# Kernel optimization log

Hardware: AMD Instinct MI355X
Metric: run time of the kernel (lower is better)

Reference implementation:

```python
import jax, jax.numpy as jnp
from jax import lax
import numpy as np

EPS_START, EPS_END, EPS_DECAY = 1.0, 0.05, 10000.0


def gru_step(x, h, w_ih, w_hh, b_ih, b_hh):
    # PyTorch GRUCell math; gates stacked as [r, z, n]
    gi = x @ w_ih.T + b_ih
    gh = h @ w_hh.T + b_hh
    i_r, i_z, i_n = jnp.split(gi, 3, axis=1)
    h_r, h_z, h_n = jnp.split(gh, 3, axis=1)
    r = jax.nn.sigmoid(i_r + h_r)
    z = jax.nn.sigmoid(i_z + h_z)
    n = jnp.tanh(i_n + r * h_n)
    return (1.0 - z) * n + z * h


def setup_inputs() -> dict:
    key = jax.random.key(0)
    ks = jax.random.split(key, 7)
    V, E, H = 32000, 256, 512
    s = 0.05
    return {
        "embedding": jax.random.normal(ks[0], (V, E), jnp.float32) * s,
        "w_ih": jax.random.normal(ks[1], (3 * H, E), jnp.float32) * s,
        "w_hh": jax.random.normal(ks[2], (3 * H, H), jnp.float32) * s,
        "b_ih": jax.random.normal(ks[3], (3 * H,), jnp.float32) * s,
        "b_hh": jax.random.normal(ks[4], (3 * H,), jnp.float32) * s,
        "w_out": jax.random.normal(ks[5], (V, H), jnp.float32) * s,
        "b_out": jax.random.normal(ks[6], (V,), jnp.float32) * s,
        "seq_len": 256,
        "batch_size": 512,
    }


def reference(embedding, w_ih, w_hh, b_ih, b_hh, w_out, b_out, seq_len, batch_size):
    V, E = embedding.shape
    H = w_hh.shape[1]
    B = batch_size
    log_unif = jnp.float32(np.log(V))  # -log(vocab_size) fill for epsilon-greedy

    keys = jax.random.split(jax.random.key(42), seq_len)
    ts = jnp.arange(seq_len, dtype=jnp.float32)

    h0 = jnp.zeros((B, H), jnp.float32)
    x0 = jnp.broadcast_to(embedding[0], (B, E))  # start token id 0

    def step(carry, inp):
        h, x = carry
        t, k = inp
        k_eps, k_gum = jax.random.split(k)
        h = gru_step(x, h, w_ih, w_hh, b_ih, b_hh)
        logp = jax.nn.log_softmax(h @ w_out.T + b_out, axis=1)  # [B, V]
        eps_t = EPS_END + (EPS_START - EPS_END) * jnp.exp(-4.0 * t / EPS_DECAY)
        draw = eps_t >= jax.random.uniform(k_eps, (B,))
        masked = jnp.where(draw[:, None], -log_unif, logp)
        g = jax.random.gumbel(k_gum, (B, V), jnp.float32)
        sampled = jnp.argmax(masked + g, axis=1)  # [B] int
        lp = jnp.take_along_axis(logp, sampled[:, None], axis=1)[:, 0]
        x_next = embedding[sampled]
        return (h, x_next), (sampled, lp)

    _, (samples, lps) = lax.scan(step, (h0, x0), (ts, keys))
    return samples.T, lps.T  # [B, S] each
```

## Files before the change

kernel.cpp:

```cpp
#include <hip/hip_runtime.h>
#include <math.h>
#include <stdio.h>

#ifndef JAX_PARTITIONABLE
#define JAX_PARTITIONABLE 1
#endif

namespace {

constexpr int B  = 512;
constexpr int S  = 256;
constexpr int E  = 256;
constexpr int H  = 512;
constexpr int V  = 32000;
constexpr int G3 = 3 * H;
constexpr int VBLK = 64;
constexpr int NCH  = V / VBLK;
constexpr int NDMAX = 96;

typedef __bf16 bf16x8 __attribute__((ext_vector_type(8)));
typedef float  f32x4  __attribute__((ext_vector_type(4)));
typedef unsigned u32x4 __attribute__((ext_vector_type(4)));

__device__ __forceinline__ void tf2x32(unsigned k0, unsigned k1,
                                       unsigned x0, unsigned x1,
                                       unsigned& o0, unsigned& o1) {
  unsigned ks2 = k0 ^ k1 ^ 0x1BD11BDAu;
  x0 += k0; x1 += k1;
#define TFR(r) { x0 += x1; x1 = (x1 << (r)) | (x1 >> (32 - (r))); x1 ^= x0; }
  TFR(13) TFR(15) TFR(26) TFR(6)   x0 += k1;  x1 += ks2 + 1u;
  TFR(17) TFR(29) TFR(16) TFR(24)  x0 += ks2; x1 += k0 + 2u;
  TFR(13) TFR(15) TFR(26) TFR(6)   x0 += k0;  x1 += k1 + 3u;
  TFR(17) TFR(29) TFR(16) TFR(24)  x0 += k1;  x1 += ks2 + 4u;
  TFR(13) TFR(15) TFR(26) TFR(6)   x0 += ks2; x1 += k0 + 5u;
#undef TFR
  o0 = x0; o1 = x1;
}

__device__ __forceinline__ unsigned rbits(unsigned g0, unsigned g1,
                                          unsigned b, unsigned v) {
#if JAX_PARTITIONABLE
  unsigned y0, y1;
  tf2x32(g0, g1, 0u, b * (unsigned)V + v, y0, y1);
  return y0 ^ y1;
#else
  const unsigned N2 = (unsigned)(B/2) * (unsigned)V;
  unsigned ii = b * (unsigned)V + v;
  unsigned jj = (b < 256) ? ii : ii - N2;
  unsigned y0, y1;
  tf2x32(g0, g1, jj, N2 + jj, y0, y1);
  return (b < 256) ? y0 : y1;
#endif
}

__device__ __forceinline__ float u01_from_bits(unsigned bits) {
  return __uint_as_float(0x3f800000u | (bits >> 9)) - 1.0f;
}

__device__ __forceinline__ float gumbel_exact(unsigned bits) {
  float u = u01_from_bits(bits);
  if (u == 0.0f) u = 1.1754943508222875e-38f;
  float w = (float)(-log((double)u));
  return (float)(-log((double)w));
}

__device__ __forceinline__ float gumbel_fast(unsigned bits) {
  float u = u01_from_bits(bits);
  if (u == 0.0f) u = 1.1754943508222875e-38f;
  float w = -__logf(u);
  return -__logf(w);
}

__device__ __forceinline__ unsigned short f2bf(float f) {
  unsigned u = __float_as_uint(f);
  unsigned r = (u + 0x7fffu + ((u >> 16) & 1u)) >> 16;
  return (unsigned short)r;
}

__device__ __forceinline__ size_t frag_off(int row, int k, int kTiles) {
  return ((size_t)((row >> 4) * kTiles + (k >> 5)) * 64
          + (row & 15) + 16 * ((k >> 3) & 3)) * 8 + (k & 7);
}

__global__ void k_init_rng(unsigned* __restrict__ kq, unsigned* __restrict__ ke) {
  int t = threadIdx.x;
  unsigned h0, h1, e0, e1, g0, g1;
#if JAX_PARTITIONABLE
  tf2x32(0u, 42u, 0u, (unsigned)t, h0, h1);
  tf2x32(h0, h1, 0u, 0u, e0, e1);
  tf2x32(h0, h1, 0u, 1u, g0, g1);
#else
  unsigned a0, a1, b0, b1;
  if (t < 128) {
    tf2x32(0u, 42u, (unsigned)(2*t),   (unsigned)(256+2*t), a0, a1);
    tf2x32(0u, 42u, (unsigned)(2*t+1), (unsigned)(257+2*t), b0, b1);
    h0 = a0; h1 = b0;
  } else {
    int j = 2*t - 256;
    tf2x32(0u, 42u, (unsigned)j,     (unsigned)(256+j), a0, a1);
    tf2x32(0u, 42u, (unsigned)(j+1), (unsigned)(257+j), b0, b1);
    h0 = a1; h1 = b1;
  }
  unsigned p0, p1, q0, q1;
  tf2x32(h0, h1, 0u, 2u, p0, p1);
  tf2x32(h0, h1, 1u, 3u, q0, q1);
  e0 = p0; e1 = q0; g0 = p1; g1 = q1;
#endif
  ke[2*t] = e0; ke[2*t+1] = e1;
  kq[2*t] = g0; kq[2*t+1] = g1;
}

__global__ void k_init_draws(const unsigned* __restrict__ ke,
                             unsigned char* __restrict__ draws) {
  int t = blockIdx.x;
  int b = threadIdx.x;
  unsigned k0 = ke[2*t], k1 = ke[2*t+1];
  unsigned bits, y0, y1;
#if JAX_PARTITIONABLE
  tf2x32(k0, k1, 0u, (unsigned)b, y0, y1);
  bits = y0 ^ y1;
#else
  if (b < 256) { tf2x32(k0, k1, (unsigned)b,       (unsigned)(256+b), y0, y1); bits = y0; }
  else         { tf2x32(k0, k1, (unsigned)(b-256), (unsigned)b,       y0, y1); bits = y1; }
#endif
  float u   = u01_from_bits(bits);
  float tf  = (float)t;
  float ex  = expf(__fmul_rn(-4.0f, tf) / 10000.0f);
  float eps = __fadd_rn(0.05f, __fmul_rn(0.95f, ex));
  draws[t*B + b] = (eps >= u) ? 1 : 0;
}

__global__ void k_init_nd(const unsigned char* __restrict__ draws,
                          int* __restrict__ nd_slot) {
  int t = blockIdx.x;
  if (threadIdx.x != 0) return;
  int cnt = 0;
  for (int b = 0; b < B; b++) {
    if (!draws[t*B + b] && cnt < NDMAX) nd_slot[t*B + b] = cnt++;
    else nd_slot[t*B + b] = -1;
  }
}

__global__ __launch_bounds__(256) void k_pre_argmax(
    const unsigned* __restrict__ kq, const unsigned char* __restrict__ draws,
    int* __restrict__ pre) {
  const int job  = blockIdx.x * 4 + (threadIdx.x >> 6);
  const int lane = threadIdx.x & 63;
  const int t = job >> 9, b = job & (B - 1);
  if (!draws[t*B + b]) { if (lane == 0) pre[job] = -1; return; }
  const unsigned g0 = kq[2*t], g1 = kq[2*t+1];
  unsigned best = 0u; int bv = V;
  for (int v = lane; v < V; v += 64) {
    unsigned bits = rbits(g0, g1, (unsigned)b, (unsigned)v) >> 9;
    if (bits > best || (bits == best && v < bv)) { best = bits; bv = v; }
  }
#pragma unroll
  for (int m = 1; m < 64; m <<= 1) {
    unsigned ob = __shfl_xor(best, m, 64);
    int      ov = __shfl_xor(bv,   m, 64);
    if (ob > best || (ob == best && ov < bv)) { best = ob; bv = ov; }
  }
  if (lane == 0) pre[job] = bv;
}

__global__ void k_init_state(const float* __restrict__ emb,
                             float* __restrict__ x, float* __restrict__ h) {
  int b = blockIdx.x, tid = threadIdx.x;
  x[b*E + tid] = emb[tid];
  h[b*H + tid] = 0.0f;
  h[b*H + 256 + tid] = 0.0f;
}

__global__ void k_cast_w(const float* __restrict__ w,
                         unsigned short* __restrict__ w_sw) {
  int g = blockIdx.x*256 + threadIdx.x;
  int v  = g >> 6;
  int k0 = (g & 63) * 8;
  const float* src = w + (size_t)v*H + k0;
  union { unsigned short s[8]; u32x4 vv; } u;
#pragma unroll
  for (int e = 0; e < 8; e++) u.s[e] = f2bf(src[e]);
  *(u32x4*)&w_sw[frag_off(v, k0, H/32)] = u.vv;
}

__global__ __launch_bounds__(512) void k_gates(
    const float* __restrict__ x, const float* __restrict__ h,
    const float* __restrict__ w_ih, const float* __restrict__ w_hh,
    const float* __restrict__ b_ih, const float* __restrict__ b_hh,
    float* __restrict__ gi, float* __restrict__ gh) {
  const int z = blockIdx.z;
  const float* A    = z ? h    : x;
  const float* W    = z ? w_hh : w_ih;
  const float* bias = z ? b_hh : b_ih;
  float*       C    = z ? gh   : gi;
  const int K       = z ? H    : E;

  __shared__ __align__(16) float As[16][68];
  __shared__ __align__(16) float Ws[16][68];
  const int tid = threadIdx.x;
  const int tx = tid & 15, ty = tid >> 4;
  const int row0 = blockIdx.y * 64, col0 = blockIdx.x * 64;
  float acc[2][4] = {};
  for (int k0 = 0; k0 < K; k0 += 16) {
#pragma unroll
    for (int l = 0; l < 2; l++) {
      int idx = tid + l*512;
      int r = idx >> 4, kk = idx & 15;
      As[kk][r] = A[(row0 + r)*K + k0 + kk];
      Ws[kk][r] = W[(col0 + r)*K + k0 + kk];
    }
    __syncthreads();
#pragma unroll
    for (int kk = 0; kk < 16; kk++) {
      const float2 av = *(const float2*)&As[kk][ty*2];
      const float4 wv = *(const float4*)&Ws[kk][tx*4];
      const float a[2] = {av.x, av.y};
      const float w[4] = {wv.x, wv.y, wv.z, wv.w};
#pragma unroll
      for (int i = 0; i < 2; i++)
#pragma unroll
        for (int j = 0; j < 4; j++) acc[i][j] = fmaf(a[i], w[j], acc[i][j]);
    }
    __syncthreads();
  }
#pragma unroll
  for (int i = 0; i < 2; i++) {
    int r = row0 + ty*2 + i;
    int c = col0 + tx*4;
    float4 o;
    o.x = __fadd_rn(acc[i][0], bias[c + 0]);
    o.y = __fadd_rn(acc[i][1], bias[c + 1]);
    o.z = __fadd_rn(acc[i][2], bias[c + 2]);
    o.w = __fadd_rn(acc[i][3], bias[c + 3]);
    *(float4*)&C[r*G3 + c] = o;
  }
}

__device__ __forceinline__ float sigm_acc(float v) {
  return (float)(1.0 / (1.0 + exp(-(double)v)));
}
__device__ __forceinline__ float tanh_acc(float v) {
  return (float)tanh((double)v);
}

__global__ void k_gru_update(const float* __restrict__ gi,
                             const float* __restrict__ gh,
                             float* __restrict__ h,
                             unsigned short* __restrict__ h_sw) {
  int g = blockIdx.x*256 + threadIdx.x;
  int b  = g >> 6;
  int j0 = (g & 63) * 8;
  const float* gib = gi + (size_t)b*G3;
  const float* ghb = gh + (size_t)b*G3;
  float hn[8];
  union { unsigned short s[8]; u32x4 vv; } u;
#pragma unroll
  for (int e = 0; e < 8; e++) {
    int j = j0 + e;
    float r  = sigm_acc(__fadd_rn(gib[j],     ghb[j]));
    float zz = sigm_acc(__fadd_rn(gib[H+j],   ghb[H+j]));
    float nn = tanh_acc(__fadd_rn(gib[2*H+j], __fmul_rn(r, ghb[2*H+j])));
    float hv = h[(size_t)b*H + j];
    float t1 = __fmul_rn(__fsub_rn(1.0f, zz), nn);
    float t2 = __fmul_rn(zz, hv);
    hn[e] = __fadd_rn(t1, t2);
    u.s[e] = f2bf(hn[e]);
  }
#pragma unroll
  for (int e = 0; e < 8; e++) h[(size_t)b*H + j0 + e] = hn[e];
  *(u32x4*)&h_sw[frag_off(b, j0, H/32)] = u.vv;
}

__global__ __launch_bounds__(256) void k_mfma_logits(
    const unsigned short* __restrict__ h_sw,
    const unsigned short* __restrict__ w_sw,
    const float* __restrict__ b_out,
    const unsigned* __restrict__ kq,
    const unsigned char* __restrict__ draws,
    int* __restrict__ pre,
    const int* __restrict__ nd_slot_t,
    float* __restrict__ pmax, float* __restrict__ psum,
    float* __restrict__ plog,
    float* __restrict__ nd_keys, float* __restrict__ nd_kmax, int t) {
  const int tid  = threadIdx.x;

  if (blockIdx.y == 0) {
    __shared__ unsigned sb[4];
    __shared__ int      sv[4];
    const int tn = t + 1;
    if (tn >= S) return;
    const int b = blockIdx.x;
    if (!draws[tn*B + b]) { if (tid == 0) pre[tn*B + b] = -1; return; }
    const unsigned g0 = kq[2*tn], g1 = kq[2*tn+1];
    unsigned best = 0u; int bv = V;
    for (int v = tid; v < V; v += 256) {
      unsigned bits = rbits(g0, g1, (unsigned)b, (unsigned)v) >> 9;
      if (bits > best || (bits == best && v < bv)) { best = bits; bv = v; }
    }
#pragma unroll
    for (int m = 1; m < 64; m <<= 1) {
      unsigned ob = __shfl_xor(best, m, 64);
      int      ov = __shfl_xor(bv,   m, 64);
      if (ob > best || (ob == best && ov < bv)) { best = ob; bv = ov; }
    }
    const int wv = tid >> 6;
    if ((tid & 63) == 0) { sb[wv] = best; sv[wv] = bv; }
    __syncthreads();
    if (tid == 0) {
      for (int i = 1; i < 4; i++) {
        unsigned ob = sb[i]; int ov = sv[i];
        if (ob > best || (ob == best && ov < bv)) { best = ob; bv = ov; }
      }
      pre[tn*B + b] = bv;
    }
    return;
  }

  const int L  = (blockIdx.y - 1) * 512 + blockIdx.x;
  const int wg = (L & 7) * 128 + (L >> 3);
  if (wg >= 2*NCH) return;
  const int vblk = wg >> 1;
  const int bblk = wg & 1;
  const int* __restrict__ pre_t = pre + t*B;
  const int lane = tid & 63, w = tid >> 6;
  const int quad = lane >> 4, l15 = lane & 15;

  f32x4 acc[4][4] = {};

  const int mtBase = bblk*16 + w*4;
  const int ntBase = vblk*4;
  const unsigned short* hp = h_sw + (size_t)mtBase*16*512 + lane*8;
  const unsigned short* wp = w_sw + (size_t)ntBase*16*512 + lane*8;

  bf16x8 afc[4], bfc[4];
#pragma unroll
  for (int mt = 0; mt < 4; mt++)
    afc[mt] = __builtin_bit_cast(bf16x8, *(const u32x4*)(hp + (size_t)(mt*16)*512));
#pragma unroll
  for (int nt = 0; nt < 4; nt++)
    bfc[nt] = __builtin_bit_cast(bf16x8, *(const u32x4*)(wp + (size_t)(nt*16)*512));

#pragma unroll 1
  for (int kt = 0; kt < 15; kt++) {
    bf16x8 afn[4], bfn[4];
#pragma unroll
    for (int mt = 0; mt < 4; mt++)
      afn[mt] = __builtin_bit_cast(bf16x8,
          *(const u32x4*)(hp + (size_t)(mt*16 + kt + 1)*512));
#pragma unroll
    for (int nt = 0; nt < 4; nt++)
      bfn[nt] = __builtin_bit_cast(bf16x8,
          *(const u32x4*)(wp + (size_t)(nt*16 + kt + 1)*512));
#pragma unroll
    for (int mt = 0; mt < 4; mt++)
#pragma unroll
      for (int nt = 0; nt < 4; nt++)
        acc[mt][nt] = __builtin_amdgcn_mfma_f32_16x16x32_bf16(
            afc[mt], bfc[nt], acc[mt][nt], 0, 0, 0);
#pragma unroll
    for (int mt = 0; mt < 4; mt++) afc[mt] = afn[mt];
#pragma unroll
    for (int nt = 0; nt < 4; nt++) bfc[nt] = bfn[nt];
  }
  {
#pragma unroll
    for (int mt = 0; mt < 4; mt++)
#pragma unroll
      for (int nt = 0; nt < 4; nt++)
        acc[mt][nt] = __builtin_amdgcn_mfma_f32_16x16x32_bf16(
            afc[mt], bfc[nt], acc[mt][nt], 0, 0, 0);
  }

  const int bW = bblk*256 + w*64;
  const int vW = vblk*64;
  const unsigned g0 = kq[2*t], g1 = kq[2*t+1];
  float bias[4];
#pragma unroll
  for (int nt = 0; nt < 4; nt++) bias[nt] = b_out[vW + nt*16 + l15];

#pragma unroll
  for (int mt = 0; mt < 4; mt++) {
#pragma unroll
    for (int r = 0; r < 4; r++) {
      const int b = bW + mt*16 + quad*4 + r;
      float lg[4];
#pragma unroll
      for (int nt = 0; nt < 4; nt++) lg[nt] = acc[mt][nt][r] + bias[nt];
      float lmax = fmaxf(fmaxf(lg[0], lg[1]), fmaxf(lg[2], lg[3]));
#pragma unroll
      for (int m = 1; m < 16; m <<= 1) lmax = fmaxf(lmax, __shfl_xor(lmax, m, 64));
      float ls = 0.0f;
#pragma unroll
      for (int nt = 0; nt < 4; nt++) ls += __expf(lg[nt] - lmax);
#pragma unroll
      for (int m = 1; m < 16; m <<= 1) ls += __shfl_xor(ls, m, 64);
      if (l15 == 0) { pmax[b*NCH + vblk] = lmax; psum[b*NCH + vblk] = ls; }
      const int pr = pre_t[b];
      if (pr >= 0) {
        int rel = pr - vW;
        if (rel >= 0 && rel < 64 && (rel & 15) == l15) plog[b] = lg[rel >> 4];
      } else {
        const int slot = nd_slot_t[b];
        if (slot >= 0) {
          float key[4];
#pragma unroll
          for (int nt = 0; nt < 4; nt++)
            key[nt] = lg[nt] + gumbel_fast(
                rbits(g0, g1, (unsigned)b, (unsigned)(vW + nt*16 + l15)));
          float* dst = nd_keys + (size_t)slot*V + vW + l15;
#pragma unroll
          for (int nt = 0; nt < 4; nt++) dst[nt*16] = key[nt];
          float kmx = fmaxf(fmaxf(key[0], key[1]), fmaxf(key[2], key[3]));
#pragma unroll
          for (int m = 1; m < 16; m <<= 1) kmx = fmaxf(kmx, __shfl_xor(kmx, m, 64));
          if (l15 == 0) nd_kmax[slot*NCH + vblk] = kmx;
        }
      }
    }
  }
}

__global__ __launch_bounds__(256) void k_finish(
    const float* __restrict__ pmax, const float* __restrict__ psum,
    const float* __restrict__ plog,
    const int* __restrict__ pre_t, const int* __restrict__ nd_slot_t,
    const float* __restrict__ nd_keys, const float* __restrict__ nd_kmax,
    const unsigned* __restrict__ kq,
    const float* __restrict__ h, const float* __restrict__ w_out,
    const float* __restrict__ b_out,
    const float* __restrict__ emb, float* __restrict__ x,
    float* __restrict__ out_samples, float* __restrict__ out_lps, int t) {
  const int b = blockIdx.x;
  const int tid = threadIdx.x;
  __shared__ float sA[256];
  __shared__ int   cand[160];
  __shared__ float cand_key[160], cand_lg[160];
  __shared__ int   ccnt;
  __shared__ int   s_samp;
  __shared__ float s_blog;

  float m = -INFINITY;
  for (int c = tid; c < NCH; c += 256) m = fmaxf(m, pmax[b*NCH + c]);
  sA[tid] = m; __syncthreads();
  for (int s = 128; s > 0; s >>= 1) {
    if (tid < s) sA[tid] = fmaxf(sA[tid], sA[tid+s]);
    __syncthreads();
  }
  const float M = sA[0];
  __syncthreads();
  float sum = 0.0f;
  for (int c = tid; c < NCH; c += 256)
    sum += psum[b*NCH + c] * expf(pmax[b*NCH + c] - M);
  sA[tid] = sum; __syncthreads();
  for (int s = 128; s > 0; s >>= 1) {
    if (tid < s) sA[tid] += sA[tid+s];
    __syncthreads();
  }
  const float SUM = sA[0];
  __syncthreads();

  const int pr = pre_t[b];
  if (pr >= 0) {
    if (tid == 0) { s_samp = pr; s_blog = plog[b]; }
  } else {
    const int slot = nd_slot_t[b];
    if (slot < 0) {
      if (tid == 0) { s_samp = 0; s_blog = plog[b]; }
    } else {
      const unsigned g0 = kq[2*t], g1 = kq[2*t+1];
      if (tid == 0) ccnt = 0;
      float km = -INFINITY;
      for (int c = tid; c < NCH; c += 256) km = fmaxf(km, nd_kmax[slot*NCH + c]);
      sA[tid] = km; __syncthreads();
      for (int s = 128; s > 0; s >>= 1) {
        if (tid < s) sA[tid] = fmaxf(sA[tid], sA[tid+s]);
        __syncthreads();
      }
      const float thr = sA[0] - 0.0859375f;
      __syncthreads();
      const float* keys = nd_keys + (size_t)slot*V;
      for (int c = tid; c < NCH; c += 256) {
        if (nd_kmax[slot*NCH + c] >= thr) {
          for (int j = 0; j < VBLK; j++) {
            float k = keys[c*VBLK + j];
            if (k >= thr) {
              int p = atomicAdd(&ccnt, 1);
              if (p < 160) cand[p] = c*VBLK + j;
            }
          }
        }
      }
      __syncthreads();
      const int nc = min(ccnt, 160);
      const int wid = tid >> 6, lane = tid & 63;
      for (int c = wid; c < nc; c += 4) {
        const int v = cand[c];
        const float* wr = w_out + (size_t)v*H;
        const float* hr = h + (size_t)b*H;
        float s = 0.0f;
#pragma unroll
        for (int i = 0; i < 8; i++) s = fmaf(hr[lane + 64*i], wr[lane + 64*i], s);
#pragma unroll
        for (int mm = 1; mm < 64; mm <<= 1) s += __shfl_xor(s, mm, 64);
        if (lane == 0) {
          float logit = __fadd_rn(s, b_out[v]);
          float key   = __fadd_rn(logit,
                          gumbel_exact(rbits(g0, g1, (unsigned)b, (unsigned)v)));
          cand_key[c] = key; cand_lg[c] = logit;
        }
      }
      __syncthreads();
      if (tid == 0) {
        float bk = -INFINITY; int bv = V; float bl = 0.0f;
        for (int c = 0; c < nc; c++) {
          float k = cand_key[c]; int v = cand[c];
          if (k > bk || (k == bk && v < bv)) { bk = k; bv = v; bl = cand_lg[c]; }
        }
        s_samp = bv; s_blog = bl;
      }
    }
  }
  __syncthreads();
  const int sampled = s_samp;
  if (tid == 0) {
    float lse = (float)log((double)SUM);
    float lp  = __fsub_rn(__fsub_rn(s_blog, M), lse);
    out_samples[b*S + t] = (float)sampled;
    out_lps[b*S + t]     = lp;
  }
  x[b*E + tid] = emb[sampled*E + tid];
}

}

extern "C" void kernel_launch(void* const* d_in, const int* in_sizes, int n_in,
                              void* d_out, int out_size, void* d_ws, size_t ws_size,
                              hipStream_t stream) {
  (void)in_sizes; (void)n_in; (void)out_size;
  const float* emb   = (const float*)d_in[0];
  const float* w_ih  = (const float*)d_in[1];
  const float* w_hh  = (const float*)d_in[2];
  const float* b_ih  = (const float*)d_in[3];
  const float* b_hh  = (const float*)d_in[4];
  const float* w_out = (const float*)d_in[5];
  const float* b_out = (const float*)d_in[6];
  float* out = (float*)d_out;

  char* wsb = (char*)d_ws;
  size_t off = 0;
  auto alloc = [&](size_t nbytes) {
    char* p = wsb + off;
    off += (nbytes + 255) & ~size_t(255);
    return p;
  };
  float* h     = (float*)alloc((size_t)B*H*4);
  float* x     = (float*)alloc((size_t)B*E*4);
  float* gi    = (float*)alloc((size_t)B*G3*4);
  float* gh    = (float*)alloc((size_t)B*G3*4);
  unsigned short* h_sw = (unsigned short*)alloc((size_t)B*H*2);
  unsigned short* w_sw = (unsigned short*)alloc((size_t)V*H*2);
  float* pmax  = (float*)alloc((size_t)B*NCH*4);
  float* psum  = (float*)alloc((size_t)B*NCH*4);
  float* plog  = (float*)alloc((size_t)B*4);
  unsigned* kq = (unsigned*)alloc((size_t)S*2*4);
  unsigned* ke = (unsigned*)alloc((size_t)S*2*4);
  unsigned char* draws = (unsigned char*)alloc((size_t)S*B);
  int* pre     = (int*)alloc((size_t)S*B*4);
  int* nd_slot = (int*)alloc((size_t)S*B*4);
  float* nd_keys = (float*)alloc((size_t)NDMAX*V*4);
  float* nd_kmax = (float*)alloc((size_t)NDMAX*NCH*4);
  if (off > ws_size) {
    fprintf(stderr, "kernel_launch: workspace too small (need %zu, have %zu)\n",
            off, ws_size);
    return;
  }

  k_init_rng<<<1, S, 0, stream>>>(kq, ke);
  k_init_draws<<<S, B, 0, stream>>>(ke, draws);
  k_init_nd<<<S, 64, 0, stream>>>(draws, nd_slot);
  k_pre_argmax<<<B/4, 256, 0, stream>>>(kq, draws, pre);
  k_init_state<<<B, 256, 0, stream>>>(emb, x, h);
  k_cast_w<<<(V*H/8)/256, 256, 0, stream>>>(w_out, w_sw);

  for (int t = 0; t < S; t++) {
    k_gates<<<dim3(G3/64, B/64, 2), 512, 0, stream>>>(x, h, w_ih, w_hh,
                                                      b_ih, b_hh, gi, gh);
    k_gru_update<<<(B*H/8)/256, 256, 0, stream>>>(gi, gh, h, h_sw);
    k_mfma_logits<<<dim3(512, 3), 256, 0, stream>>>(
        h_sw, w_sw, b_out, kq, draws, pre, nd_slot + t*B,
        pmax, psum, plog, nd_keys, nd_kmax, t);
    k_finish<<<B, 256, 0, stream>>>(pmax, psum, plog, pre + t*B, nd_slot + t*B,
                                    nd_keys, nd_kmax, kq, h, w_out, b_out,
                                    emb, x, out, out + (size_t)B*S, t);
  }
}
```

Before: 35.87 ms.

## Fuse GRU gate GEMMs with the GRU update and ping-pong hidden state

The separate gate GEMM kernel and GRU update kernel become one kernel. Each block computes the r, z and n gate columns for 8 hidden units over 64 batch rows, then applies the GRU nonlinearity directly, so the gi/gh intermediates never round-trip through global memory and one launch per step is removed. The hidden state is double-buffered so a block can read the old h while others write the new one. The cost is a smaller per-block tile (8 columns x 3 gates) with less register reuse. Each thread also writes scalar bf16 stores to the swizzled buffer instead of 16-byte vector stores.

```diff
diff --git a/kernel.cpp b/kernel.cpp
--- a/kernel.cpp
+++ b/kernel.cpp
@@ -13,7 +13,6 @@
 constexpr int E  = 256;
 constexpr int H  = 512;
 constexpr int V  = 32000;
-constexpr int G3 = 3 * H;
 constexpr int VBLK = 64;
 constexpr int NCH  = V / VBLK;
 constexpr int NDMAX = 96;
@@ -183,92 +182,107 @@
   *(u32x4*)&w_sw[frag_off(v, k0, H/32)] = u.vv;
 }
 
-__global__ __launch_bounds__(512) void k_gates(
-    const float* __restrict__ x, const float* __restrict__ h,
+__device__ __forceinline__ float sigm_acc(float v) {
+  return (float)(1.0 / (1.0 + exp(-(double)v)));
+}
+__device__ __forceinline__ float tanh_acc(float v) {
+  return (float)tanh((double)v);
+}
+
+__global__ __launch_bounds__(256) void k_gates_gru(
+    const float* __restrict__ x, const float* __restrict__ hin,
     const float* __restrict__ w_ih, const float* __restrict__ w_hh,
     const float* __restrict__ b_ih, const float* __restrict__ b_hh,
-    float* __restrict__ gi, float* __restrict__ gh) {
-  const int z = blockIdx.z;
-  const float* A    = z ? h    : x;
-  const float* W    = z ? w_hh : w_ih;
-  const float* bias = z ? b_hh : b_ih;
-  float*       C    = z ? gh   : gi;
-  const int K       = z ? H    : E;
-
+    float* __restrict__ hout, unsigned short* __restrict__ h_sw) {
   __shared__ __align__(16) float As[16][68];
-  __shared__ __align__(16) float Ws[16][68];
+  __shared__ __align__(16) float Ws[16][28];
   const int tid = threadIdx.x;
-  const int tx = tid & 15, ty = tid >> 4;
-  const int row0 = blockIdx.y * 64, col0 = blockIdx.x * 64;
-  float acc[2][4] = {};
-  for (int k0 = 0; k0 < K; k0 += 16) {
+  const int jj = tid & 7, ty = tid >> 3;
+  const int j0 = blockIdx.x * 8;
+  const int row0 = blockIdx.y * 64;
+  float ai[2][3] = {};
+  float ah[2][3] = {};
+
+  for (int k0 = 0; k0 < E; k0 += 16) {
+    __syncthreads();
+#pragma unroll
+    for (int l = 0; l < 4; l++) {
+      int idx = tid + l*256;
+      int r = idx >> 4, kk = idx & 15;
+      As[kk][r] = x[(size_t)(row0 + r)*E + k0 + kk];
+    }
 #pragma unroll
     for (int l = 0; l < 2; l++) {
-      int idx = tid + l*512;
+      int idx = tid + l*256;
+      if (idx < 384) {
+        int r = idx >> 4, kk = idx & 15;
+        int col = (r >> 3)*512 + j0 + (r & 7);
+        Ws[kk][r] = w_ih[(size_t)col*E + k0 + kk];
+      }
+    }
+    __syncthreads();
+#pragma unroll
+    for (int kk = 0; kk < 16; kk++) {
+      float a0 = As[kk][ty], a1 = As[kk][ty + 32];
+#pragma unroll
+      for (int g = 0; g < 3; g++) {
+        float w = Ws[kk][g*8 + jj];
+        ai[0][g] = fmaf(a0, w, ai[0][g]);
+        ai[1][g] = fmaf(a1, w, ai[1][g]);
+      }
+    }
+  }
+
+  for (int k0 = 0; k0 < H; k0 += 16) {
+    __syncthreads();
+#pragma unroll
+    for (int l = 0; l < 4; l++) {
+      int idx = tid + l*256;
       int r = idx >> 4, kk = idx & 15;
-      As[kk][r] = A[(row0 + r)*K + k0 + kk];
-      Ws[kk][r] = W[(col0 + r)*K + k0 + kk];
+      As[kk][r] = hin[(size_t)(row0 + r)*H + k0 + kk];
+    }
+#pragma unroll
+    for (int l = 0; l < 2; l++) {
+      int idx = tid + l*256;
+      if (idx < 384) {
+        int r = idx >> 4, kk = idx & 15;
+        int col = (r >> 3)*512 + j0 + (r & 7);
+        Ws[kk][r] = w_hh[(size_t)col*H + k0 + kk];
+      }
     }
     __syncthreads();
 #pragma unroll
     for (int kk = 0; kk < 16; kk++) {
-      const float2 av = *(const float2*)&As[kk][ty*2];
-      const float4 wv = *(const float4*)&Ws[kk][tx*4];
-      const float a[2] = {av.x, av.y};
-      const float w[4] = {wv.x, wv.y, wv.z, wv.w};
-#pragma unroll
-      for (int i = 0; i < 2; i++)
-#pragma unroll
-        for (int j = 0; j < 4; j++) acc[i][j] = fmaf(a[i], w[j], acc[i][j]);
-    }
-    __syncthreads();
-  }
+      float a0 = As[kk][ty], a1 = As[kk][ty + 32];
+#pragma unroll
+      for (int g = 0; g < 3; g++) {
+        float w = Ws[kk][g*8 + jj];
+        ah[0][g] = fmaf(a0, w, ah[0][g]);
+        ah[1][g] = fmaf(a1, w, ah[1][g]);
+      }
+    }
+  }
+
+  const int j = j0 + jj;
 #pragma unroll
   for (int i = 0; i < 2; i++) {
-    int r = row0 + ty*2 + i;
-    int c = col0 + tx*4;
-    float4 o;
-    o.x = __fadd_rn(acc[i][0], bias[c + 0]);
-    o.y = __fadd_rn(acc[i][1], bias[c + 1]);
-    o.z = __fadd_rn(acc[i][2], bias[c + 2]);
-    o.w = __fadd_rn(acc[i][3], bias[c + 3]);
-    *(float4*)&C[r*G3 + c] = o;
-  }
-}
-
-__device__ __forceinline__ float sigm_acc(float v) {
-  return (float)(1.0 / (1.0 + exp(-(double)v)));
-}
-__device__ __forceinline__ float tanh_acc(float v) {
-  return (float)tanh((double)v);
-}
-
-__global__ void k_gru_update(const float* __restrict__ gi,
-                             const float* __restrict__ gh,
-                             float* __restrict__ h,
-                             unsigned short* __restrict__ h_sw) {
-  int g = blockIdx.x*256 + threadIdx.x;
-  int b  = g >> 6;
-  int j0 = (g & 63) * 8;
-  const float* gib = gi + (size_t)b*G3;
-  const float* ghb = gh + (size_t)b*G3;
-  float hn[8];
-  union { unsigned short s[8]; u32x4 vv; } u;
-#pragma unroll
-  for (int e = 0; e < 8; e++) {
-    int j = j0 + e;
-    float r  = sigm_acc(__fadd_rn(gib[j],     ghb[j]));
-    float zz = sigm_acc(__fadd_rn(gib[H+j],   ghb[H+j]));
-    float nn = tanh_acc(__fadd_rn(gib[2*H+j], __fmul_rn(r, ghb[2*H+j])));
-    float hv = h[(size_t)b*H + j];
+    const int b = row0 + ty + i*32;
+    float gi_r = __fadd_rn(ai[i][0], b_ih[j]);
+    float gi_z = __fadd_rn(ai[i][1], b_ih[512 + j]);
+    float gi_n = __fadd_rn(ai[i][2], b_ih[1024 + j]);
+    float gh_r = __fadd_rn(ah[i][0], b_hh[j]);
+    float gh_z = __fadd_rn(ah[i][1], b_hh[512 + j]);
+    float gh_n = __fadd_rn(ah[i][2], b_hh[1024 + j]);
+    float r  = sigm_acc(__fadd_rn(gi_r, gh_r));
+    float zz = sigm_acc(__fadd_rn(gi_z, gh_z));
+    float nn = tanh_acc(__fadd_rn(gi_n, __fmul_rn(r, gh_n)));
+    float hv = hin[(size_t)b*H + j];
     float t1 = __fmul_rn(__fsub_rn(1.0f, zz), nn);
     float t2 = __fmul_rn(zz, hv);
-    hn[e] = __fadd_rn(t1, t2);
-    u.s[e] = f2bf(hn[e]);
-  }
-#pragma unroll
-  for (int e = 0; e < 8; e++) h[(size_t)b*H + j0 + e] = hn[e];
-  *(u32x4*)&h_sw[frag_off(b, j0, H/32)] = u.vv;
+    float hn = __fadd_rn(t1, t2);
+    hout[(size_t)b*H + j] = hn;
+    h_sw[frag_off(b, j, H/32)] = f2bf(hn);
+  }
 }
 
 __global__ __launch_bounds__(256) void k_mfma_logits(
@@ -553,10 +567,9 @@
     off += (nbytes + 255) & ~size_t(255);
     return p;
   };
-  float* h     = (float*)alloc((size_t)B*H*4);
+  float* h0    = (float*)alloc((size_t)B*H*4);
+  float* h1    = (float*)alloc((size_t)B*H*4);
   float* x     = (float*)alloc((size_t)B*E*4);
-  float* gi    = (float*)alloc((size_t)B*G3*4);
-  float* gh    = (float*)alloc((size_t)B*G3*4);
   unsigned short* h_sw = (unsigned short*)alloc((size_t)B*H*2);
   unsigned short* w_sw = (unsigned short*)alloc((size_t)V*H*2);
   float* pmax  = (float*)alloc((size_t)B*NCH*4);
@@ -579,18 +592,19 @@
   k_init_draws<<<S, B, 0, stream>>>(ke, draws);
   k_init_nd<<<S, 64, 0, stream>>>(draws, nd_slot);
   k_pre_argmax<<<B/4, 256, 0, stream>>>(kq, draws, pre);
-  k_init_state<<<B, 256, 0, stream>>>(emb, x, h);
+  k_init_state<<<B, 256, 0, stream>>>(emb, x, h0);
   k_cast_w<<<(V*H/8)/256, 256, 0, stream>>>(w_out, w_sw);
 
   for (int t = 0; t < S; t++) {
-    k_gates<<<dim3(G3/64, B/64, 2), 512, 0, stream>>>(x, h, w_ih, w_hh,
-                                                      b_ih, b_hh, gi, gh);
-    k_gru_update<<<(B*H/8)/256, 256, 0, stream>>>(gi, gh, h, h_sw);
+    float* hin  = (t & 1) ? h1 : h0;
+    float* hout = (t & 1) ? h0 : h1;
+    k_gates_gru<<<dim3(64, 8), 256, 0, stream>>>(x, hin, w_ih, w_hh,
+                                                 b_ih, b_hh, hout, h_sw);
     k_mfma_logits<<<dim3(512, 3), 256, 0, stream>>>(
         h_sw, w_sw, b_out, kq, draws, pre, nd_slot + t*B,
         pmax, psum, plog, nd_keys, nd_kmax, t);
     k_finish<<<B, 256, 0, stream>>>(pmax, psum, plog, pre + t*B, nd_slot + t*B,
-                                    nd_keys, nd_kmax, kq, h, w_out, b_out,
+                                    nd_keys, nd_kmax, kq, hout, w_out, b_out,
                                     emb, x, out, out + (size_t)B*S, t);
   }
 }
```

Measured after the change: 39.49 ms. 10.1% more time.

## Fuse GRU update and finish into preceding kernels via atomic last-block counters

Applied to the files above, without the earlier changes.

The GRU elementwise update moves into k_gates: the last of the 48 blocks to finish a 64-row batch slab, detected with an atomic counter, applies the gates for that slab. The finish/sampling stage moves into k_mfma_logits: the last 512 blocks to arrive spin until all blocks have written their partials, then each does the per-row reduction and sampling. This cuts two kernel launches per timestep, 512 launches in total. In exchange it needs relaxed atomic loads and stores for cross-block visibility, ping-pong h buffers, and a spin-wait whose forward progress depends on all blocks of the grid being resident or already retired.

```diff
diff --git a/kernel.cpp b/kernel.cpp
--- a/kernel.cpp
+++ b/kernel.cpp
@@ -21,6 +21,9 @@
 typedef __bf16 bf16x8 __attribute__((ext_vector_type(8)));
 typedef float  f32x4  __attribute__((ext_vector_type(4)));
 typedef unsigned u32x4 __attribute__((ext_vector_type(4)));
+
+#define AST(p, v) __hip_atomic_store((p), (v), __ATOMIC_RELAXED, __HIP_MEMORY_SCOPE_AGENT)
+#define ALD(p)    __hip_atomic_load((p), __ATOMIC_RELAXED, __HIP_MEMORY_SCOPE_AGENT)
 
 __device__ __forceinline__ void tf2x32(unsigned k0, unsigned k1,
                                        unsigned x0, unsigned x1,
@@ -82,8 +85,10 @@
           + (row & 15) + 16 * ((k >> 3) & 3)) * 8 + (k & 7);
 }
 
-__global__ void k_init_rng(unsigned* __restrict__ kq, unsigned* __restrict__ ke) {
+__global__ void k_init_rng(unsigned* __restrict__ kq, unsigned* __restrict__ ke,
+                           unsigned* __restrict__ ctrs) {
   int t = threadIdx.x;
+  ctrs[t] = 0u;
   unsigned h0, h1, e0, e1, g0, g1;
 #if JAX_PARTITIONABLE
   tf2x32(0u, 42u, 0u, (unsigned)t, h0, h1);
@@ -183,13 +188,22 @@
   *(u32x4*)&w_sw[frag_off(v, k0, H/32)] = u.vv;
 }
 
+__device__ __forceinline__ float sigm_acc(float v) {
+  return (float)(1.0 / (1.0 + exp(-(double)v)));
+}
+__device__ __forceinline__ float tanh_acc(float v) {
+  return (float)tanh((double)v);
+}
+
 __global__ __launch_bounds__(512) void k_gates(
-    const float* __restrict__ x, const float* __restrict__ h,
+    const float* __restrict__ x, const float* __restrict__ hin,
     const float* __restrict__ w_ih, const float* __restrict__ w_hh,
     const float* __restrict__ b_ih, const float* __restrict__ b_hh,
-    float* __restrict__ gi, float* __restrict__ gh) {
+    float* __restrict__ gi, float* __restrict__ gh,
+    float* __restrict__ hout, unsigned short* __restrict__ h_sw,
+    unsigned* __restrict__ ctrs, int t) {
   const int z = blockIdx.z;
-  const float* A    = z ? h    : x;
+  const float* A    = z ? hin  : x;
   const float* W    = z ? w_hh : w_ih;
   const float* bias = z ? b_hh : b_ih;
   float*       C    = z ? gh   : gi;
@@ -197,6 +211,7 @@
 
   __shared__ __align__(16) float As[16][68];
   __shared__ __align__(16) float Ws[16][68];
+  __shared__ unsigned s_old;
   const int tid = threadIdx.x;
   const int tx = tid & 15, ty = tid >> 4;
   const int row0 = blockIdx.y * 64, col0 = blockIdx.x * 64;
@@ -227,51 +242,41 @@
   for (int i = 0; i < 2; i++) {
     int r = row0 + ty*2 + i;
     int c = col0 + tx*4;
-    float4 o;
-    o.x = __fadd_rn(acc[i][0], bias[c + 0]);
-    o.y = __fadd_rn(acc[i][1], bias[c + 1]);
-    o.z = __fadd_rn(acc[i][2], bias[c + 2]);
-    o.w = __fadd_rn(acc[i][3], bias[c + 3]);
-    *(float4*)&C[r*G3 + c] = o;
-  }
-}
-
-__device__ __forceinline__ float sigm_acc(float v) {
-  return (float)(1.0 / (1.0 + exp(-(double)v)));
-}
-__device__ __forceinline__ float tanh_acc(float v) {
-  return (float)tanh((double)v);
-}
-
-__global__ void k_gru_update(const float* __restrict__ gi,
-                             const float* __restrict__ gh,
-                             float* __restrict__ h,
-                             unsigned short* __restrict__ h_sw) {
-  int g = blockIdx.x*256 + threadIdx.x;
-  int b  = g >> 6;
-  int j0 = (g & 63) * 8;
-  const float* gib = gi + (size_t)b*G3;
-  const float* ghb = gh + (size_t)b*G3;
-  float hn[8];
-  union { unsigned short s[8]; u32x4 vv; } u;
-#pragma unroll
-  for (int e = 0; e < 8; e++) {
-    int j = j0 + e;
-    float r  = sigm_acc(__fadd_rn(gib[j],     ghb[j]));
-    float zz = sigm_acc(__fadd_rn(gib[H+j],   ghb[H+j]));
-    float nn = tanh_acc(__fadd_rn(gib[2*H+j], __fmul_rn(r, ghb[2*H+j])));
-    float hv = h[(size_t)b*H + j];
+#pragma unroll
+    for (int j = 0; j < 4; j++)
+      AST(&C[(size_t)r*G3 + c + j], __fadd_rn(acc[i][j], bias[c + j]));
+  }
+
+  asm volatile("s_waitcnt vmcnt(0)" ::: "memory");
+  __syncthreads();
+  if (tid == 0)
+    s_old = __hip_atomic_fetch_add(&ctrs[blockIdx.y * 16], 1u,
+                                   __ATOMIC_RELAXED, __HIP_MEMORY_SCOPE_AGENT);
+  __syncthreads();
+  if (s_old != 48u * (unsigned)(t + 1) - 1u) return;
+
+  for (int el = tid; el < 64 * H; el += 512) {
+    const int b = row0 + (el >> 9);
+    const int j = el & (H - 1);
+    float gir = ALD(&gi[(size_t)b*G3 + j]);
+    float giz = ALD(&gi[(size_t)b*G3 + H + j]);
+    float gin = ALD(&gi[(size_t)b*G3 + 2*H + j]);
+    float ghr = ALD(&gh[(size_t)b*G3 + j]);
+    float ghz = ALD(&gh[(size_t)b*G3 + H + j]);
+    float ghn = ALD(&gh[(size_t)b*G3 + 2*H + j]);
+    float r  = sigm_acc(__fadd_rn(gir, ghr));
+    float zz = sigm_acc(__fadd_rn(giz, ghz));
+    float nn = tanh_acc(__fadd_rn(gin, __fmul_rn(r, ghn)));
+    float hv = hin[(size_t)b*H + j];
     float t1 = __fmul_rn(__fsub_rn(1.0f, zz), nn);
     float t2 = __fmul_rn(zz, hv);
-    hn[e] = __fadd_rn(t1, t2);
-    u.s[e] = f2bf(hn[e]);
-  }
-#pragma unroll
-  for (int e = 0; e < 8; e++) h[(size_t)b*H + j0 + e] = hn[e];
-  *(u32x4*)&h_sw[frag_off(b, j0, H/32)] = u.vv;
-}
-
-__global__ __launch_bounds__(256) void k_mfma_logits(
+    float hn = __fadd_rn(t1, t2);
+    hout[(size_t)b*H + j] = hn;
+    h_sw[frag_off(b, j, H/32)] = f2bf(hn);
+  }
+}
+
+__global__ __launch_bounds__(256, 2) void k_mfma_logits(
     const unsigned short* __restrict__ h_sw,
     const unsigned short* __restrict__ w_sw,
     const float* __restrict__ b_out,
@@ -281,12 +286,23 @@
     const int* __restrict__ nd_slot_t,
     float* __restrict__ pmax, float* __restrict__ psum,
     float* __restrict__ plog,
-    float* __restrict__ nd_keys, float* __restrict__ nd_kmax, int t) {
+    float* __restrict__ nd_keys, float* __restrict__ nd_kmax,
+    const float* __restrict__ h, const float* __restrict__ w_out,
+    const float* __restrict__ emb, float* __restrict__ x,
+    float* __restrict__ out_samples, float* __restrict__ out_lps,
+    unsigned* __restrict__ ctrs, int t) {
   const int tid  = threadIdx.x;
+  __shared__ unsigned sb[4];
+  __shared__ int      sv[4];
+  __shared__ unsigned s_old;
+  __shared__ float sA[256];
+  __shared__ int   cand[160];
+  __shared__ float cand_key[160], cand_lg[160];
+  __shared__ int   ccnt;
+  __shared__ int   s_samp;
+  __shared__ float s_blog;
 
   if (blockIdx.y == 0) {
-    __shared__ unsigned sb[4];
-    __shared__ int      sv[4];
     const int tn = t + 1;
     if (tn >= S) return;
     const int b = blockIdx.x;
@@ -319,216 +335,224 @@
   const int L  = (blockIdx.y - 1) * 512 + blockIdx.x;
   const int wg = (L & 7) * 128 + (L >> 3);
   if (wg >= 2*NCH) return;
-  const int vblk = wg >> 1;
-  const int bblk = wg & 1;
-  const int* __restrict__ pre_t = pre + t*B;
-  const int lane = tid & 63, w = tid >> 6;
-  const int quad = lane >> 4, l15 = lane & 15;
-
-  f32x4 acc[4][4] = {};
-
-  const int mtBase = bblk*16 + w*4;
-  const int ntBase = vblk*4;
-  const unsigned short* hp = h_sw + (size_t)mtBase*16*512 + lane*8;
-  const unsigned short* wp = w_sw + (size_t)ntBase*16*512 + lane*8;
-
-  bf16x8 afc[4], bfc[4];
-#pragma unroll
-  for (int mt = 0; mt < 4; mt++)
-    afc[mt] = __builtin_bit_cast(bf16x8, *(const u32x4*)(hp + (size_t)(mt*16)*512));
-#pragma unroll
-  for (int nt = 0; nt < 4; nt++)
-    bfc[nt] = __builtin_bit_cast(bf16x8, *(const u32x4*)(wp + (size_t)(nt*16)*512));
+  {
+    const int vblk = wg >> 1;
+    const int bblk = wg & 1;
+    const int* __restrict__ pre_t = pre + t*B;
+    const int lane = tid & 63, w = tid >> 6;
+    const int quad = lane >> 4, l15 = lane & 15;
+
+    f32x4 acc[4][4] = {};
+
+    const int mtBase = bblk*16 + w*4;
+    const int ntBase = vblk*4;
+    const unsigned short* hp = h_sw + (size_t)mtBase*16*512 + lane*8;
+    const unsigned short* wp = w_sw + (size_t)ntBase*16*512 + lane*8;
+
+    bf16x8 afc[4], bfc[4];
+#pragma unroll
+    for (int mt = 0; mt < 4; mt++)
+      afc[mt] = __builtin_bit_cast(bf16x8, *(const u32x4*)(hp + (size_t)(mt*16)*512));
+#pragma unroll
+    for (int nt = 0; nt < 4; nt++)
+      bfc[nt] = __builtin_bit_cast(bf16x8, *(const u32x4*)(wp + (size_t)(nt*16)*512));
 
 #pragma unroll 1
-  for (int kt = 0; kt < 15; kt++) {
-    bf16x8 afn[4], bfn[4];
-#pragma unroll
-    for (int mt = 0; mt < 4; mt++)
-      afn[mt] = __builtin_bit_cast(bf16x8,
-          *(const u32x4*)(hp + (size_t)(mt*16 + kt + 1)*512));
-#pragma unroll
-    for (int nt = 0; nt < 4; nt++)
-      bfn[nt] = __builtin_bit_cast(bf16x8,
-          *(const u32x4*)(wp + (size_t)(nt*16 + kt + 1)*512));
-#pragma unroll
-    for (int mt = 0; mt < 4; mt++)
+    for (int kt = 0; kt < 15; kt++) {
+      bf16x8 afn[4], bfn[4];
+#pragma unroll
+      for (int mt = 0; mt < 4; mt++)
+        afn[mt] = __builtin_bit_cast(bf16x8,
+            *(const u32x4*)(hp + (size_t)(mt*16 + kt + 1)*512));
 #pragma unroll
       for (int nt = 0; nt < 4; nt++)
-        acc[mt][nt] = __builtin_amdgcn_mfma_f32_16x16x32_bf16(
-            afc[mt], bfc[nt], acc[mt][nt], 0, 0, 0);
-#pragma unroll
-    for (int mt = 0; mt < 4; mt++) afc[mt] = afn[mt];
-#pragma unroll
-    for (int nt = 0; nt < 4; nt++) bfc[nt] = bfn[nt];
-  }
-  {
-#pragma unroll
-    for (int mt = 0; mt < 4; mt++)
-#pragma unroll
-      for (int nt = 0; nt < 4; nt++)
-        acc[mt][nt] = __builtin_amdgcn_mfma_f32_16x16x32_bf16(
-            afc[mt], bfc[nt], acc[mt][nt], 0, 0, 0);
-  }
-
-  const int bW = bblk*256 + w*64;
-  const int vW = vblk*64;
-  const unsigned g0 = kq[2*t], g1 = kq[2*t+1];
-  float bias[4];
-#pragma unroll
-  for (int nt = 0; nt < 4; nt++) bias[nt] = b_out[vW + nt*16 + l15];
-
-#pragma unroll
-  for (int mt = 0; mt < 4; mt++) {
-#pragma unroll
-    for (int r = 0; r < 4; r++) {
-      const int b = bW + mt*16 + quad*4 + r;
-      float lg[4];
-#pragma unroll
-      for (int nt = 0; nt < 4; nt++) lg[nt] = acc[mt][nt][r] + bias[nt];
-      float lmax = fmaxf(fmaxf(lg[0], lg[1]), fmaxf(lg[2], lg[3]));
-#pragma unroll
-      for (int m = 1; m < 16; m <<= 1) lmax = fmaxf(lmax, __shfl_xor(lmax, m, 64));
-      float ls = 0.0f;
-#pragma unroll
-      for (int nt = 0; nt < 4; nt++) ls += __expf(lg[nt] - lmax);
-#pragma unroll
-      for (int m = 1; m < 16; m <<= 1) ls += __shfl_xor(ls, m, 64);
-      if (l15 == 0) { pmax[b*NCH + vblk] = lmax; psum[b*NCH + vblk] = ls; }
-      const int pr = pre_t[b];
-      if (pr >= 0) {
-        int rel = pr - vW;
-        if (rel >= 0 && rel < 64 && (rel & 15) == l15) plog[b] = lg[rel >> 4];
-      } else {
-        const int slot = nd_slot_t[b];
-        if (slot >= 0) {
-          float key[4];
-#pragma unroll
-          for (int nt = 0; nt < 4; nt++)
-            key[nt] = lg[nt] + gumbel_fast(
-                rbits(g0, g1, (unsigned)b, (unsigned)(vW + nt*16 + l15)));
-          float* dst = nd_keys + (size_t)slot*V + vW + l15;
-#pragma unroll
-          for (int nt = 0; nt < 4; nt++) dst[nt*16] = key[nt];
-          float kmx = fmaxf(fmaxf(key[0], key[1]), fmaxf(key[2], key[3]));
-#pragma unroll
-          for (int m = 1; m < 16; m <<= 1) kmx = fmaxf(kmx, __shfl_xor(kmx, m, 64));
-          if (l15 == 0) nd_kmax[slot*NCH + vblk] = kmx;
+        bfn[nt] = __builtin_bit_cast(bf16x8,
+            *(const u32x4*)(wp + (size_t)(nt*16 + kt + 1)*512));
+#pragma unroll
+      for (int mt = 0; mt < 4; mt++)
+#pragma unroll
+        for (int nt = 0; nt < 4; nt++)
+          acc[mt][nt] = __builtin_amdgcn_mfma_f32_16x16x32_bf16(
+              afc[mt], bfc[nt], acc[mt][nt], 0, 0, 0);
+#pragma unroll
+      for (int mt = 0; mt < 4; mt++) afc[mt] = afn[mt];
+#pragma unroll
+      for (int nt = 0; nt < 4; nt++) bfc[nt] = bfn[nt];
+    }
+    {
+#pragma unroll
+      for (int mt = 0; mt < 4; mt++)
+#pragma unroll
+        for (int nt = 0; nt < 4; nt++)
+          acc[mt][nt] = __builtin_amdgcn_mfma_f32_16x16x32_bf16(
+              afc[mt], bfc[nt], acc[mt][nt], 0, 0, 0);
+    }
+
+    const int bW = bblk*256 + w*64;
+    const int vW = vblk*64;
+    const unsigned g0 = kq[2*t], g1 = kq[2*t+1];
+    float bias[4];
+#pragma unroll
+    for (int nt = 0; nt < 4; nt++) bias[nt] = b_out[vW + nt*16 + l15];
+
+#pragma unroll
+    for (int mt = 0; mt < 4; mt++) {
+#pragma unroll
+      for (int r = 0; r < 4; r++) {
+        const int b = bW + mt*16 + quad*4 + r;
+        float lg[4];
+#pragma unroll
+        for (int nt = 0; nt < 4; nt++) lg[nt] = acc[mt][nt][r] + bias[nt];
+        float lmax = fmaxf(fmaxf(lg[0], lg[1]), fmaxf(lg[2], lg[3]));
+#pragma unroll
+        for (int m = 1; m < 16; m <<= 1) lmax = fmaxf(lmax, __shfl_xor(lmax, m, 64));
+        float ls = 0.0f;
+#pragma unroll
+        for (int nt = 0; nt < 4; nt++) ls += __expf(lg[nt] - lmax);
+#pragma unroll
+        for (int m = 1; m < 16; m <<= 1) ls += __shfl_xor(ls, m, 64);
+        if (l15 == 0) {
+          AST(&pmax[b*NCH + vblk], lmax);
+          AST(&psum[b*NCH + vblk], ls);
+        }
+        const int pr = pre_t[b];
+        if (pr >= 0) {
+          int rel = pr - vW;
+          if (rel >= 0 && rel < 64 && (rel & 15) == l15)
+            AST(&plog[b], lg[rel >> 4]);
+        } else {
+          const int slot = nd_slot_t[b];
+          if (slot >= 0) {
+            float key[4];
+#pragma unroll
+            for (int nt = 0; nt < 4; nt++)
+              key[nt] = lg[nt] + gumbel_fast(
+                  rbits(g0, g1, (unsigned)b, (unsigned)(vW + nt*16 + l15)));
+            float* dst = nd_keys + (size_t)slot*V + vW + l15;
+#pragma unroll
+            for (int nt = 0; nt < 4; nt++) AST(&dst[nt*16], key[nt]);
+            float kmx = fmaxf(fmaxf(key[0], key[1]), fmaxf(key[2], key[3]));
+#pragma unroll
+            for (int m = 1; m < 16; m <<= 1) kmx = fmaxf(kmx, __shfl_xor(kmx, m, 64));
+            if (l15 == 0) AST(&nd_kmax[slot*NCH + vblk], kmx);
+          }
         }
       }
     }
   }
-}
-
-__global__ __launch_bounds__(256) void k_finish(
-    const float* __restrict__ pmax, const float* __restrict__ psum,
-    const float* __restrict__ plog,
-    const int* __restrict__ pre_t, const int* __restrict__ nd_slot_t,
-    const float* __restrict__ nd_keys, const float* __restrict__ nd_kmax,
-    const unsigned* __restrict__ kq,
-    const float* __restrict__ h, const float* __restrict__ w_out,
-    const float* __restrict__ b_out,
-    const float* __restrict__ emb, float* __restrict__ x,
-    float* __restrict__ out_samples, float* __restrict__ out_lps, int t) {
-  const int b = blockIdx.x;
-  const int tid = threadIdx.x;
-  __shared__ float sA[256];
-  __shared__ int   cand[160];
-  __shared__ float cand_key[160], cand_lg[160];
-  __shared__ int   ccnt;
-  __shared__ int   s_samp;
-  __shared__ float s_blog;
-
-  float m = -INFINITY;
-  for (int c = tid; c < NCH; c += 256) m = fmaxf(m, pmax[b*NCH + c]);
-  sA[tid] = m; __syncthreads();
-  for (int s = 128; s > 0; s >>= 1) {
-    if (tid < s) sA[tid] = fmaxf(sA[tid], sA[tid+s]);
+
+  asm volatile("s_waitcnt vmcnt(0)" ::: "memory");
+  __syncthreads();
+  if (tid == 0)
+    s_old = __hip_atomic_fetch_add(&ctrs[128], 1u,
+                                   __ATOMIC_RELAXED, __HIP_MEMORY_SCOPE_AGENT);
+  __syncthreads();
+  const unsigned base = 1000u * (unsigned)t;
+  if (s_old < base + 488u) return;
+  const int fb = (int)(s_old - (base + 488u));
+  if (tid == 0) {
+    while (__hip_atomic_load(&ctrs[128], __ATOMIC_RELAXED,
+                             __HIP_MEMORY_SCOPE_AGENT) < base + 1000u)
+      __builtin_amdgcn_s_sleep(2);
+  }
+  __syncthreads();
+
+  {
+    const int b = fb;
+    const int* pre_t    = pre + t*B;
+
+    float m = -INFINITY;
+    for (int c = tid; c < NCH; c += 256) m = fmaxf(m, ALD(&pmax[b*NCH + c]));
+    sA[tid] = m; __syncthreads();
+    for (int s = 128; s > 0; s >>= 1) {
+      if (tid < s) sA[tid] = fmaxf(sA[tid], sA[tid+s]);
+      __syncthreads();
+    }
+    const float M = sA[0];
     __syncthreads();
-  }
-  const float M = sA[0];
-  __syncthreads();
-  float sum = 0.0f;
-  for (int c = tid; c < NCH; c += 256)
-    sum += psum[b*NCH + c] * expf(pmax[b*NCH + c] - M);
-  sA[tid] = sum; __syncthreads();
-  for (int s = 128; s > 0; s >>= 1) {
-    if (tid < s) sA[tid] += sA[tid+s];
+    float sum = 0.0f;
+    for (int c = tid; c < NCH; c += 256)
+      sum += ALD(&psum[b*NCH + c]) * expf(ALD(&pmax[b*NCH + c]) - M);
+    sA[tid] = sum; __syncthreads();
+    for (int s = 128; s > 0; s >>= 1) {
+      if (tid < s) sA[tid] += sA[tid+s];
+      __syncthreads();
+    }
+    const float SUM = sA[0];
     __syncthreads();
-  }
-  const float SUM = sA[0];
-  __syncthreads();
-
-  const int pr = pre_t[b];
-  if (pr >= 0) {
-    if (tid == 0) { s_samp = pr; s_blog = plog[b]; }
-  } else {
-    const int slot = nd_slot_t[b];
-    if (slot < 0) {
-      if (tid == 0) { s_samp = 0; s_blog = plog[b]; }
+
+    const int pr = pre_t[b];
+    if (pr >= 0) {
+      if (tid == 0) { s_samp = pr; s_blog = ALD(&plog[b]); }
     } else {
-      const unsigned g0 = kq[2*t], g1 = kq[2*t+1];
-      if (tid == 0) ccnt = 0;
-      float km = -INFINITY;
-      for (int c = tid; c < NCH; c += 256) km = fmaxf(km, nd_kmax[slot*NCH + c]);
-      sA[tid] = km; __syncthreads();
-      for (int s = 128; s > 0; s >>= 1) {
-        if (tid < s) sA[tid] = fmaxf(sA[tid], sA[tid+s]);
+      const int slot = nd_slot_t[b];
+      if (slot < 0) {
+        if (tid == 0) { s_samp = 0; s_blog = ALD(&plog[b]); }
+      } else {
+        const unsigned g0 = kq[2*t], g1 = kq[2*t+1];
+        if (tid == 0) ccnt = 0;
+        float km = -INFINITY;
+        for (int c = tid; c < NCH; c += 256)
+          km = fmaxf(km, ALD(&nd_kmax[slot*NCH + c]));
+        sA[tid] = km; __syncthreads();
+        for (int s = 128; s > 0; s >>= 1) {
+          if (tid < s) sA[tid] = fmaxf(sA[tid], sA[tid+s]);
+          __syncthreads();
+        }
+        const float thr = sA[0] - 0.0859375f;
         __syncthreads();
-      }
-      const float thr = sA[0] - 0.0859375f;
-      __syncthreads();
-      const float* keys = nd_keys + (size_t)slot*V;
-      for (int c = tid; c < NCH; c += 256) {
-        if (nd_kmax[slot*NCH + c] >= thr) {
-          for (int j = 0; j < VBLK; j++) {
-            float k = keys[c*VBLK + j];
-            if (k >= thr) {
-              int p = atomicAdd(&ccnt, 1);
-              if (p < 160) cand[p] = c*VBLK + j;
+        float* keys = nd_keys + (size_t)slot*V;
+        for (int c = tid; c < NCH; c += 256) {
+          if (ALD(&nd_kmax[slot*NCH + c]) >= thr) {
+            for (int j = 0; j < VBLK; j++) {
+              float k = ALD(&keys[c*VBLK + j]);
+              if (k >= thr) {
+                int p = atomicAdd(&ccnt, 1);
+                if (p < 160) cand[p] = c*VBLK + j;
+              }
             }
           }
         }
-      }
-      __syncthreads();
-      const int nc = min(ccnt, 160);
-      const int wid = tid >> 6, lane = tid & 63;
-      for (int c = wid; c < nc; c += 4) {
-        const int v = cand[c];
-        const float* wr = w_out + (size_t)v*H;
-        const float* hr = h + (size_t)b*H;
-        float s = 0.0f;
-#pragma unroll
-        for (int i = 0; i < 8; i++) s = fmaf(hr[lane + 64*i], wr[lane + 64*i], s);
-#pragma unroll
-        for (int mm = 1; mm < 64; mm <<= 1) s += __shfl_xor(s, mm, 64);
-        if (lane == 0) {
-          float logit = __fadd_rn(s, b_out[v]);
-          float key   = __fadd_rn(logit,
-                          gumbel_exact(rbits(g0, g1, (unsigned)b, (unsigned)v)));
-          cand_key[c] = key; cand_lg[c] = logit;
+        __syncthreads();
+        const int nc = min(ccnt, 160);
+        const int wid = tid >> 6, lane = tid & 63;
+        for (int c = wid; c < nc; c += 4) {
+          const int v = cand[c];
+          const float* wr = w_out + (size_t)v*H;
+          const float* hr = h + (size_t)b*H;
+          float s = 0.0f;
+#pragma unroll
+          for (int i = 0; i < 8; i++) s = fmaf(hr[lane + 64*i], wr[lane + 64*i], s);
+#pragma unroll
+          for (int mm = 1; mm < 64; mm <<= 1) s += __shfl_xor(s, mm, 64);
+          if (lane == 0) {
+            float logit = __fadd_rn(s, b_out[v]);
+            float key   = __fadd_rn(logit,
+                            gumbel_exact(rbits(g0, g1, (unsigned)b, (unsigned)v)));
+            cand_key[c] = key; cand_lg[c] = logit;
+          }
+        }
+        __syncthreads();
+        if (tid == 0) {
+          float bk = -INFINITY; int bv = V; float bl = 0.0f;
+          for (int c = 0; c < nc; c++) {
+            float k = cand_key[c]; int v = cand[c];
+            if (k > bk || (k == bk && v < bv)) { bk = k; bv = v; bl = cand_lg[c]; }
+          }
+          s_samp = bv; s_blog = bl;
         }
       }
-      __syncthreads();
-      if (tid == 0) {
-        float bk = -INFINITY; int bv = V; float bl = 0.0f;
-        for (int c = 0; c < nc; c++) {
-          float k = cand_key[c]; int v = cand[c];
-          if (k > bk || (k == bk && v < bv)) { bk = k; bv = v; bl = cand_lg[c]; }
-        }
-        s_samp = bv; s_blog = bl;
-      }
-    }
-  }
-  __syncthreads();
-  const int sampled = s_samp;
-  if (tid == 0) {
-    float lse = (float)log((double)SUM);
-    float lp  = __fsub_rn(__fsub_rn(s_blog, M), lse);
-    out_samples[b*S + t] = (float)sampled;
-    out_lps[b*S + t]     = lp;
-  }
-  x[b*E + tid] = emb[sampled*E + tid];
+    }
+    __syncthreads();
+    const int sampled = s_samp;
+    if (tid == 0) {
+      float lse = (float)log((double)SUM);
+      float lp  = __fsub_rn(__fsub_rn(s_blog, M), lse);
+      out_samples[b*S + t] = (float)sampled;
+      out_lps[b*S + t]     = lp;
+    }
+    x[b*E + tid] = emb[sampled*E + tid];
+  }
 }
 
 }
@@ -553,7 +577,8 @@
     off += (nbytes + 255) & ~size_t(255);
     return p;
   };
-  float* h     = (float*)alloc((size_t)B*H*4);
+  float* h0    = (float*)alloc((size_t)B*H*4);
+  float* h1    = (float*)alloc((size_t)B*H*4);
   float* x     = (float*)alloc((size_t)B*E*4);
   float* gi    = (float*)alloc((size_t)B*G3*4);
   float* gh    = (float*)alloc((size_t)B*G3*4);
@@ -569,28 +594,28 @@
   int* nd_slot = (int*)alloc((size_t)S*B*4);
   float* nd_keys = (float*)alloc((size_t)NDMAX*V*4);
   float* nd_kmax = (float*)alloc((size_t)NDMAX*NCH*4);
+  unsigned* ctrs = (unsigned*)alloc(256*4);
   if (off > ws_size) {
     fprintf(stderr, "kernel_launch: workspace too small (need %zu, have %zu)\n",
             off, ws_size);
     return;
   }
 
-  k_init_rng<<<1, S, 0, stream>>>(kq, ke);
+  k_init_rng<<<1, S, 0, stream>>>(kq, ke, ctrs);
   k_init_draws<<<S, B, 0, stream>>>(ke, draws);
   k_init_nd<<<S, 64, 0, stream>>>(draws, nd_slot);
   k_pre_argmax<<<B/4, 256, 0, stream>>>(kq, draws, pre);
-  k_init_state<<<B, 256, 0, stream>>>(emb, x, h);
+  k_init_state<<<B, 256, 0, stream>>>(emb, x, h0);
   k_cast_w<<<(V*H/8)/256, 256, 0, stream>>>(w_out, w_sw);
 
   for (int t = 0; t < S; t++) {
-    k_gates<<<dim3(G3/64, B/64, 2), 512, 0, stream>>>(x, h, w_ih, w_hh,
-                                                      b_ih, b_hh, gi, gh);
-    k_gru_update<<<(B*H/8)/256, 256, 0, stream>>>(gi, gh, h, h_sw);
+    float* hin  = (t & 1) ? h1 : h0;
+    float* hout = (t & 1) ? h0 : h1;
+    k_gates<<<dim3(G3/64, B/64, 2), 512, 0, stream>>>(
+        x, hin, w_ih, w_hh, b_ih, b_hh, gi, gh, hout, h_sw, ctrs, t);
     k_mfma_logits<<<dim3(512, 3), 256, 0, stream>>>(
         h_sw, w_sw, b_out, kq, draws, pre, nd_slot + t*B,
-        pmax, psum, plog, nd_keys, nd_kmax, t);
-    k_finish<<<B, 256, 0, stream>>>(pmax, psum, plog, pre + t*B, nd_slot + t*B,
-                                    nd_keys, nd_kmax, kq, h, w_out, b_out,
-                                    emb, x, out, out + (size_t)B*S, t);
-  }
-}
+        pmax, psum, plog, nd_keys, nd_kmax,
+        hout, w_out, emb, x, out, out + (size_t)B*S, ctrs, t);
+  }
+}
```

New measurement: 62.01 ms. 72.9% more time.
